# Performance work log

Measured on AMD Instinct MI355X. Metric: run time of the kernel, lower is better.

The kernel has to match this reference:

```python
import jax, jax.numpy as jnp
import numpy as np

BATCH = 4096
DIM = 256
TEMP = 0.5
COS_EPS = 1e-8  # torch.nn.CosineSimilarity default eps


def setup_inputs() -> dict:
    key = jax.random.key(0)
    k1, k2 = jax.random.split(key)
    zis = jax.random.normal(k1, (BATCH, DIM), dtype=jnp.float32)
    zjs = jax.random.normal(k2, (BATCH, DIM), dtype=jnp.float32)
    return {"zis": zis, "zjs": zjs}


def reference(zis, zjs):
    n = zis.shape[0]  # batch_size
    # representations = cat([zjs, zis]) -> (2N, D)
    reps = jnp.concatenate([zjs, zis], axis=0)
    # cosine similarity matrix: dot / max(|x||y|, eps)  (matches torch CosineSimilarity)
    norms = jnp.linalg.norm(reps, axis=-1)  # (2N,)
    sim = (reps @ reps.T) / jnp.maximum(norms[:, None] * norms[None, :], COS_EPS)  # (2N, 2N)
    # positives: diag at offset +N (rows 0..N-1) then offset -N (rows N..2N-1)
    pos = jnp.concatenate([jnp.diagonal(sim, n), jnp.diagonal(sim, -n)])  # (2N,)
    # CE with label 0 over [pos, negatives]: negatives = row minus {diag, positive};
    # logsumexp([pos] + negatives) == logsumexp(row with only the self-diagonal masked),
    # since the positive appears exactly once in the row.
    two_n = 2 * n
    logits = sim / TEMP
    logits = jnp.where(jnp.eye(two_n, dtype=bool), -jnp.inf, logits)
    lse = jax.nn.logsumexp(logits, axis=-1)  # (2N,)
    loss = jnp.sum(lse - pos / TEMP)  # CrossEntropyLoss(reduction='sum')
    return loss / two_n
```

## Files before the change

kernel.cpp:

```cpp
#include <hip/hip_runtime.h>
#include <hip/hip_bf16.h>

#define TWO_N  8192
#define N_HALF 4096
#define DIMS   256

typedef __bf16 bf16x8 __attribute__((ext_vector_type(8)));
typedef float  f32x4  __attribute__((ext_vector_type(4)));
typedef unsigned short ushort8v __attribute__((ext_vector_type(8)));

__device__ __forceinline__ float fast_exp2(float x) {
#if __has_builtin(__builtin_amdgcn_exp2f)
    return __builtin_amdgcn_exp2f(x);
#else
    float r; asm("v_exp_f32 %0, %1" : "=v"(r) : "v"(x)); return r;
#endif
}

__global__ __launch_bounds__(256) void nrm_kernel(const float* __restrict__ zis,
                                                  const float* __restrict__ zjs,
                                                  unsigned short* __restrict__ swz)
{
    const int tid = threadIdx.x;
    const int l32 = tid & 31;
    const int row = blockIdx.x * 8 + (tid >> 5);
    const int k0  = l32 * 8;

    const float* src = (row < N_HALF) ? (zjs + (size_t)row * DIMS)
                                      : (zis + (size_t)(row - N_HALF) * DIMS);
    const float4 v0 = reinterpret_cast<const float4*>(src + k0)[0];
    const float4 v1 = reinterpret_cast<const float4*>(src + k0 + 4)[0];
    float ss = v0.x * v0.x + v0.y * v0.y + v0.z * v0.z + v0.w * v0.w
             + v1.x * v1.x + v1.y * v1.y + v1.z * v1.z + v1.w * v1.w;
#pragma unroll
    for (int m = 1; m < 32; m <<= 1) ss += __shfl_xor(ss, m, 64);
    const float inv = rsqrtf(ss) * 1.69864360045f;

    const float vals[8] = {v0.x, v0.y, v0.z, v0.w, v1.x, v1.y, v1.z, v1.w};
    ushort8v o;
#pragma unroll
    for (int j = 0; j < 8; ++j) {
        __hip_bfloat16 b = __float2bfloat16(vals[j] * inv);
        o[j] = *reinterpret_cast<unsigned short*>(&b);
    }
    const int chunk = ((row >> 4) * 8 + (l32 >> 2)) * 64 + (l32 & 3) * 16 + (row & 15);
    *reinterpret_cast<ushort8v*>(swz + (size_t)chunk * 8) = o;
}

__global__ __launch_bounds__(256, 2) void ntx_kernel(const __bf16* __restrict__ swz,
                                                     float* __restrict__ rowsum_part,
                                                     float* __restrict__ pos_part)
{
    const int lane = threadIdx.x & 63;
    const int wave = threadIdx.x >> 6;
    const int l15  = lane & 15;
    const int quad = lane >> 4;

    const int rg     = blockIdx.x & 31;
    const int cs     = blockIdx.x >> 5;
    const int wr0    = rg * 256 + wave * 64;
    const int c_base = cs * 256;
    const int p0     = wr0 ^ N_HALF;

    bf16x8 bfrag[4][8];
#pragma unroll
    for (int t = 0; t < 4; ++t) {
        const __bf16* bp = swz + (size_t)((wr0 >> 4) + t) * 4096 + lane * 8;
#pragma unroll
        for (int kk = 0; kk < 8; ++kk)
            bfrag[t][kk] = *reinterpret_cast<const bf16x8*>(bp + kk * 512);
    }

    const __bf16* abase = swz + (size_t)(cs * 16) * 4096 + lane * 8;

    float sum_exp[4] = {0.f, 0.f, 0.f, 0.f};
    float pos_acc = 0.f;

    bf16x8 a0[8], a1[8];
#pragma unroll
    for (int kk = 0; kk < 8; ++kk)
        a0[kk] = *reinterpret_cast<const bf16x8*>(abase + kk * 512);

    auto compute = [&](const bf16x8* af, int it) {
        const int c0 = c_base + it * 16;
        f32x4 acc[4] = {{0.f, 0.f, 0.f, 0.f}, {0.f, 0.f, 0.f, 0.f},
                        {0.f, 0.f, 0.f, 0.f}, {0.f, 0.f, 0.f, 0.f}};
#pragma unroll
        for (int kk = 0; kk < 8; ++kk) {
#pragma unroll
            for (int t = 0; t < 4; ++t)
                acc[t] = __builtin_amdgcn_mfma_f32_16x16x32_bf16(
                    af[kk], bfrag[t][kk], acc[t], 0, 0, 0);
        }
        const bool special = (c0 < wr0 + 64 && c0 + 16 > wr0) ||
                             (c0 < p0 + 64 && c0 + 16 > p0);
        if (!special) {
#pragma unroll
            for (int t = 0; t < 4; ++t)
#pragma unroll
                for (int j = 0; j < 4; ++j)
                    sum_exp[t] += fast_exp2(acc[t][j]);
        } else {
#pragma unroll
            for (int t = 0; t < 4; ++t) {
                const int r = wr0 + t * 16 + l15;
#pragma unroll
                for (int j = 0; j < 4; ++j) {
                    const int c = c0 + quad * 4 + j;
                    const float e = fast_exp2(acc[t][j]);
                    sum_exp[t] += (c == r) ? 0.f : e;
                    if (c == (r ^ N_HALF)) pos_acc += acc[t][j];
                }
            }
        }
    };

    for (int it = 0; it < 16; it += 2) {
#pragma unroll
        for (int kk = 0; kk < 8; ++kk)
            a1[kk] = *reinterpret_cast<const bf16x8*>(abase + (size_t)(it + 1) * 4096 + kk * 512);
        compute(a0, it);
        if (it + 2 < 16) {
#pragma unroll
            for (int kk = 0; kk < 8; ++kk)
                a0[kk] = *reinterpret_cast<const bf16x8*>(abase + (size_t)(it + 2) * 4096 + kk * 512);
        }
        compute(a1, it + 1);
    }

#pragma unroll
    for (int t = 0; t < 4; ++t) {
        float s = sum_exp[t];
        s += __shfl_xor(s, 16, 64);
        s += __shfl_xor(s, 32, 64);
        if (lane < 16)
            rowsum_part[(size_t)cs * TWO_N + wr0 + t * 16 + lane] = s;
    }

#pragma unroll
    for (int m = 1; m < 64; m <<= 1) pos_acc += __shfl_xor(pos_acc, m, 64);
    if (lane == 0) pos_part[blockIdx.x * 4 + wave] = pos_acc;
}

__global__ __launch_bounds__(1024) void fin1_kernel(const float* __restrict__ rowsum_part,
                                                    const float* __restrict__ pos_part,
                                                    float* __restrict__ block_part)
{
    __shared__ float red[16];
    const int t = threadIdx.x;
    const int r = blockIdx.x * 1024 + t;
    float acc = 0.f;
#pragma unroll
    for (int cs = 0; cs < 32; ++cs)
        acc += rowsum_part[(size_t)cs * TWO_N + r];
    float v = logf(acc);
    if (t < 512)
        v -= 0.69314718055994531f * pos_part[blockIdx.x * 512 + t];
#pragma unroll
    for (int m = 1; m < 64; m <<= 1) v += __shfl_xor(v, m, 64);
    if ((t & 63) == 0) red[t >> 6] = v;
    __syncthreads();
    if (t == 0) {
        float s = 0.f;
#pragma unroll
        for (int w = 0; w < 16; ++w) s += red[w];
        block_part[blockIdx.x] = s;
    }
}

__global__ void fin2_kernel(const float* __restrict__ block_part, float* __restrict__ out)
{
    if (threadIdx.x == 0) {
        float s = 0.f;
#pragma unroll
        for (int i = 0; i < 8; ++i) s += block_part[i];
        out[0] = s / (float)TWO_N;
    }
}

extern "C" void kernel_launch(void* const* d_in, const int* in_sizes, int n_in,
                              void* d_out, int out_size, void* d_ws, size_t ws_size,
                              hipStream_t stream)
{
    const float* zis = (const float*)d_in[0];
    const float* zjs = (const float*)d_in[1];

    unsigned short* swz = (unsigned short*)d_ws;
    float* rowsum_part  = (float*)((char*)d_ws + (size_t)TWO_N * DIMS * sizeof(unsigned short));
    float* pos_part     = rowsum_part + (size_t)32 * TWO_N;
    float* block_part   = pos_part + 4096;

    nrm_kernel<<<TWO_N / 8, 256, 0, stream>>>(zis, zjs, swz);
    ntx_kernel<<<1024, 256, 0, stream>>>((const __bf16*)swz, rowsum_part, pos_part);
    fin1_kernel<<<8, 1024, 0, stream>>>(rowsum_part, pos_part, block_part);
    fin2_kernel<<<1, 64, 0, stream>>>(block_part, (float*)d_out);
}
```

Baseline: 94.78 us.

## Halve per-wave row tile and drop A double-buffering for higher occupancy

Each wave now owns 32 rows (two 16-row MFMA tiles) instead of 64, so the grid doubles to 2048 blocks and launch bounds ask for 4 blocks per CU. The explicit double-buffered A-fragment prefetch is replaced by a simple per-iteration load, which cuts VGPR use and lets more waves hide latency. The cost is that each A fragment is reused across only two B tiles instead of four, doubling A-fragment global/L2 traffic. The pos_part buffer and the fin1 reduction are resized to match the doubled partial count.

```diff
diff --git a/kernel.cpp b/kernel.cpp
--- a/kernel.cpp
+++ b/kernel.cpp
@@ -47,7 +47,7 @@
     *reinterpret_cast<ushort8v*>(swz + (size_t)chunk * 8) = o;
 }
 
-__global__ __launch_bounds__(256, 2) void ntx_kernel(const __bf16* __restrict__ swz,
+__global__ __launch_bounds__(256, 4) void ntx_kernel(const __bf16* __restrict__ swz,
                                                      float* __restrict__ rowsum_part,
                                                      float* __restrict__ pos_part)
 {
@@ -56,15 +56,15 @@
     const int l15  = lane & 15;
     const int quad = lane >> 4;
 
-    const int rg     = blockIdx.x & 31;
-    const int cs     = blockIdx.x >> 5;
-    const int wr0    = rg * 256 + wave * 64;
+    const int rg     = blockIdx.x & 63;
+    const int cs     = blockIdx.x >> 6;
+    const int wr0    = rg * 128 + wave * 32;
     const int c_base = cs * 256;
     const int p0     = wr0 ^ N_HALF;
 
-    bf16x8 bfrag[4][8];
+    bf16x8 bfrag[2][8];
 #pragma unroll
-    for (int t = 0; t < 4; ++t) {
+    for (int t = 0; t < 2; ++t) {
         const __bf16* bp = swz + (size_t)((wr0 >> 4) + t) * 4096 + lane * 8;
 #pragma unroll
         for (int kk = 0; kk < 8; ++kk)
@@ -73,36 +73,35 @@
 
     const __bf16* abase = swz + (size_t)(cs * 16) * 4096 + lane * 8;
 
-    float sum_exp[4] = {0.f, 0.f, 0.f, 0.f};
+    float sum_exp[2] = {0.f, 0.f};
     float pos_acc = 0.f;
 
-    bf16x8 a0[8], a1[8];
+    for (int it = 0; it < 16; ++it) {
+        bf16x8 a[8];
 #pragma unroll
-    for (int kk = 0; kk < 8; ++kk)
-        a0[kk] = *reinterpret_cast<const bf16x8*>(abase + kk * 512);
+        for (int kk = 0; kk < 8; ++kk)
+            a[kk] = *reinterpret_cast<const bf16x8*>(abase + (size_t)it * 4096 + kk * 512);
 
-    auto compute = [&](const bf16x8* af, int it) {
         const int c0 = c_base + it * 16;
-        f32x4 acc[4] = {{0.f, 0.f, 0.f, 0.f}, {0.f, 0.f, 0.f, 0.f},
-                        {0.f, 0.f, 0.f, 0.f}, {0.f, 0.f, 0.f, 0.f}};
+        f32x4 acc[2] = {{0.f, 0.f, 0.f, 0.f}, {0.f, 0.f, 0.f, 0.f}};
 #pragma unroll
         for (int kk = 0; kk < 8; ++kk) {
 #pragma unroll
-            for (int t = 0; t < 4; ++t)
+            for (int t = 0; t < 2; ++t)
                 acc[t] = __builtin_amdgcn_mfma_f32_16x16x32_bf16(
-                    af[kk], bfrag[t][kk], acc[t], 0, 0, 0);
+                    a[kk], bfrag[t][kk], acc[t], 0, 0, 0);
         }
-        const bool special = (c0 < wr0 + 64 && c0 + 16 > wr0) ||
-                             (c0 < p0 + 64 && c0 + 16 > p0);
+        const bool special = (c0 < wr0 + 32 && c0 + 16 > wr0) ||
+                             (c0 < p0 + 32 && c0 + 16 > p0);
         if (!special) {
 #pragma unroll
-            for (int t = 0; t < 4; ++t)
+            for (int t = 0; t < 2; ++t)
 #pragma unroll
                 for (int j = 0; j < 4; ++j)
                     sum_exp[t] += fast_exp2(acc[t][j]);
         } else {
 #pragma unroll
-            for (int t = 0; t < 4; ++t) {
+            for (int t = 0; t < 2; ++t) {
                 const int r = wr0 + t * 16 + l15;
 #pragma unroll
                 for (int j = 0; j < 4; ++j) {
@@ -113,23 +112,10 @@
                 }
             }
         }
-    };
-
-    for (int it = 0; it < 16; it += 2) {
-#pragma unroll
-        for (int kk = 0; kk < 8; ++kk)
-            a1[kk] = *reinterpret_cast<const bf16x8*>(abase + (size_t)(it + 1) * 4096 + kk * 512);
-        compute(a0, it);
-        if (it + 2 < 16) {
-#pragma unroll
-            for (int kk = 0; kk < 8; ++kk)
-                a0[kk] = *reinterpret_cast<const bf16x8*>(abase + (size_t)(it + 2) * 4096 + kk * 512);
-        }
-        compute(a1, it + 1);
     }
 
 #pragma unroll
-    for (int t = 0; t < 4; ++t) {
+    for (int t = 0; t < 2; ++t) {
         float s = sum_exp[t];
         s += __shfl_xor(s, 16, 64);
         s += __shfl_xor(s, 32, 64);
@@ -153,9 +139,7 @@
 #pragma unroll
     for (int cs = 0; cs < 32; ++cs)
         acc += rowsum_part[(size_t)cs * TWO_N + r];
-    float v = logf(acc);
-    if (t < 512)
-        v -= 0.69314718055994531f * pos_part[blockIdx.x * 512 + t];
+    float v = logf(acc) - 0.69314718055994531f * pos_part[r];
 #pragma unroll
     for (int m = 1; m < 64; m <<= 1) v += __shfl_xor(v, m, 64);
     if ((t & 63) == 0) red[t >> 6] = v;
@@ -188,10 +172,10 @@
     unsigned short* swz = (unsigned short*)d_ws;
     float* rowsum_part  = (float*)((char*)d_ws + (size_t)TWO_N * DIMS * sizeof(unsigned short));
     float* pos_part     = rowsum_part + (size_t)32 * TWO_N;
-    float* block_part   = pos_part + 4096;
+    float* block_part   = pos_part + TWO_N;
 
     nrm_kernel<<<TWO_N / 8, 256, 0, stream>>>(zis, zjs, swz);
-    ntx_kernel<<<1024, 256, 0, stream>>>((const __bf16*)swz, rowsum_part, pos_part);
+    ntx_kernel<<<2048, 256, 0, stream>>>((const __bf16*)swz, rowsum_part, pos_part);
     fin1_kernel<<<8, 1024, 0, stream>>>(rowsum_part, pos_part, block_part);
     fin2_kernel<<<1, 64, 0, stream>>>(block_part, (float*)d_out);
 }
```

New measurement: 105.2 us. +10.9%, slower.
